# Kernel optimization log

Hardware: AMD Instinct MI355X
Metric: run time of the kernel (lower is better)

Reference implementation:

```python
import jax, jax.numpy as jnp
import numpy as np
import math

# LLaMA-7B-style int8 attention (torch-int Int8LlamaAttention)
B, S, HID, NH, HD = 2, 1024, 4096, 32, 128
THETA = 10000.0
# per-tensor quantization scales (as produced by from_float)
S_IN, S_W, S_B = 0.02, 0.01, 0.1
S_Q, S_K, S_V, S_O = 0.05, 0.05, 0.05, 0.05


def _rope_tables(position_ids):
    inv_freq = 1.0 / (THETA ** (jnp.arange(0, HD, 2, dtype=jnp.float32) / HD))
    freqs = position_ids.astype(jnp.float32)[..., None] * inv_freq  # [B,S,HD//2]
    emb = jnp.concatenate([freqs, freqs], axis=-1)  # [B,S,HD]
    return jnp.cos(emb)[:, None], jnp.sin(emb)[:, None]  # [B,1,S,HD]


def _rotate_half(x):
    return jnp.concatenate([-x[..., HD // 2:], x[..., :HD // 2]], axis=-1)


def _quant_i8(x):
    return jnp.clip(jnp.round(x), -128, 127).astype(jnp.int8)


def _w8a8b8o8(x_i8, w_i8, b_i8, alpha, beta):
    # int8 GEMM with int32 accumulation, fused dequant-requant to int8
    acc = jnp.einsum('bsk,nk->bsn', x_i8.astype(jnp.int32), w_i8.astype(jnp.int32))
    return _quant_i8(acc.astype(jnp.float32) * alpha + b_i8.astype(jnp.float32) * beta)


def setup_inputs() -> dict:
    key = jax.random.key(0)
    ks = jax.random.split(key, 9)
    ri8 = lambda k, shp: jax.random.randint(k, shp, -127, 128, dtype=jnp.int8)
    return {
        'hidden_states': jax.random.normal(ks[0], (B, S, HID), jnp.float32),
        'position_ids': jnp.broadcast_to(jnp.arange(S, dtype=jnp.int32), (B, S)),
        'w_q': ri8(ks[1], (HID, HID)),
        'w_k': ri8(ks[2], (HID, HID)),
        'w_v': ri8(ks[3], (HID, HID)),
        'w_o': ri8(ks[4], (HID, HID)),
        'b_q': ri8(ks[5], (HID,)),
        'b_k': ri8(ks[6], (HID,)),
        'b_v': ri8(ks[7], (HID,)),
        'b_o': jax.random.normal(ks[8], (HID,), jnp.float32) * 0.01,
    }


def reference(hidden_states, position_ids, w_q, w_k, w_v, w_o, b_q, b_k, b_v, b_o):
    # quantize activations, run int8 q/k/v projections (W8A8B8O8Linear)
    x_i8 = _quant_i8(hidden_states / S_IN)
    q = _w8a8b8o8(x_i8, w_q, b_q, S_IN * S_W / S_Q, S_B / S_Q)
    k = _w8a8b8o8(x_i8, w_k, b_k, S_IN * S_W / S_K, S_B / S_K)
    v = _w8a8b8o8(x_i8, w_v, b_v, S_IN * S_W / S_V, S_B / S_V)
    to_heads = lambda t: t.reshape(B, S, NH, HD).transpose(0, 2, 1, 3)  # [B,NH,S,HD]
    q, k, v = to_heads(q), to_heads(k), to_heads(v)
    # RoPE applied on dequantized int8 values, requantized for the int8 qk bmm
    cos, sin = _rope_tables(position_ids)
    qf, kf = q.astype(jnp.float32), k.astype(jnp.float32)
    q_i8 = _quant_i8(qf * cos + _rotate_half(qf) * sin)
    k_i8 = _quant_i8(kf * cos + _rotate_half(kf) * sin)
    # BMM_S8T_S8N_F32T: int8 QK^T -> fp32 with scale s_q*s_k, then /sqrt(d)
    attn = jnp.einsum('bhsd,bhtd->bhst', q_i8.astype(jnp.int32), k_i8.astype(jnp.int32))
    attn = attn.astype(jnp.float32) * (S_Q * S_K) / math.sqrt(HD)
    # NOTE: source never applies the attention mask (`attn_weights = attn_weights`)
    p = jax.nn.softmax(attn, axis=-1)
    # probs quantized to int8 with scale 1/127 for BMM_S8T_S8N_S8T
    p_i8 = _quant_i8(p * 127.0)
    ctx = jnp.einsum('bhst,bhtd->bhsd', p_i8.astype(jnp.int32), v.astype(jnp.int32))
    ctx_i8 = _quant_i8(ctx.astype(jnp.float32) * ((1.0 / 127.0) * S_V / S_O))
    ctx_i8 = ctx_i8.transpose(0, 2, 1, 3).reshape(B, S, HID)
    # W8A8BFP32OFP32 o_proj: int8 GEMM, fp32 output + fp32 bias
    out = jnp.einsum('bsk,nk->bsn', ctx_i8.astype(jnp.int32), w_o.astype(jnp.int32))
    return out.astype(jnp.float32) * (S_O * S_W) + b_o
```

## Files before the change

### kernel.cpp

```cpp
#include <hip/hip_runtime.h>
#include <hip/hip_bf16.h>
#include <cstdint>
#include <cstddef>

typedef int v4i __attribute__((ext_vector_type(4)));

#define NH 32
#define HD 128
#define SEQ 1024
#define HID 4096
#define BB 2
#define BKB 128

__device__ __forceinline__ signed char quant_i8(float x) {
    float r = rintf(x);
    r = fminf(fmaxf(r, -128.0f), 127.0f);
    return (signed char)r;
}

#define GLOAD_LDS16(g, l) \
    __builtin_amdgcn_global_load_lds((const __attribute__((address_space(1))) void*)(g), \
                                     (__attribute__((address_space(3))) void*)(l), 16, 0, 0)

__global__ __launch_bounds__(256) void pack4_i8_kernel(
    const int* __restrict__ s0, const int* __restrict__ s1,
    const int* __restrict__ s2, const int* __restrict__ s3,
    signed char* __restrict__ d0, signed char* __restrict__ d1,
    signed char* __restrict__ d2, signed char* __restrict__ d3, int n4)
{
    int i = blockIdx.x * 256 + threadIdx.x;
    int which = i / n4;
    int idx = i - which * n4;
    const int* src = (which == 0) ? s0 : (which == 1) ? s1 : (which == 2) ? s2 : s3;
    signed char* dst = (which == 0) ? d0 : (which == 1) ? d1 : (which == 2) ? d2 : d3;
    int4 v = ((const int4*)src)[idx];
    char4 c;
    c.x = (signed char)v.x; c.y = (signed char)v.y;
    c.z = (signed char)v.z; c.w = (signed char)v.w;
    ((char4*)dst)[idx] = c;
}

__global__ __launch_bounds__(256) void quant_x_kernel(const float* __restrict__ src,
                                                      signed char* __restrict__ dst, int n4) {
    int i = blockIdx.x * 256 + threadIdx.x;
    if (i >= n4) return;
    float4 v = ((const float4*)src)[i];
    char4 c;
    c.x = quant_i8(v.x * 50.0f);
    c.y = quant_i8(v.y * 50.0f);
    c.z = quant_i8(v.z * 50.0f);
    c.w = quant_i8(v.w * 50.0f);
    ((char4*)dst)[i] = c;
}

template<bool F32OUT>
__device__ __forceinline__ void gemm_core_db(
    const signed char* __restrict__ A, const signed char* __restrict__ Bw,
    const void* __restrict__ bias, void* __restrict__ outp,
    int m0, int n0, int N, int K, float alpha, float beta)
{
    __shared__ __align__(16) signed char sA[2 * 128 * BKB];
    __shared__ __align__(16) signed char sB[2 * 128 * BKB];

    const int t    = threadIdx.x;
    const int w    = t >> 6;
    const int lane = t & 63;
    const int lm   = lane & 15;
    const int quad = lane >> 4;
    const int wm   = (w >> 1) * 64;
    const int wn   = (w & 1) * 64;

    int srow[4], skc[4];
    #pragma unroll
    for (int p = 0; p < 4; p++) {
        int si = t + 256 * p;
        int row = si >> 3;
        srow[p] = row;
        skc[p] = ((si & 7) - (row >> 1)) & 7;
    }

    v4i acc[4][4] = {};

    #pragma unroll
    for (int p = 0; p < 4; p++) {
        GLOAD_LDS16(A  + (size_t)(m0 + srow[p]) * K + skc[p] * 16, sA + t * 16 + p * 4096);
        GLOAD_LDS16(Bw + (size_t)(n0 + srow[p]) * K + skc[p] * 16, sB + t * 16 + p * 4096);
    }

    int buf = 0;
    for (int k0 = 0; k0 < K; k0 += BKB) {
        __syncthreads();

        if (k0 + BKB < K) {
            int nb = buf ^ 1;
            #pragma unroll
            for (int p = 0; p < 4; p++) {
                GLOAD_LDS16(A  + (size_t)(m0 + srow[p]) * K + k0 + BKB + skc[p] * 16,
                            sA + nb * 16384 + t * 16 + p * 4096);
                GLOAD_LDS16(Bw + (size_t)(n0 + srow[p]) * K + k0 + BKB + skc[p] * 16,
                            sB + nb * 16384 + t * 16 + p * 4096);
            }
        }

        const signed char* pA = sA + buf * 16384;
        const signed char* pB = sB + buf * 16384;
        #pragma unroll
        for (int ks = 0; ks < 2; ks++) {
            v4i af[4], bf[4];
            #pragma unroll
            for (int i = 0; i < 4; i++) {
                int row = wm + 16 * i + lm;
                int slot = (ks * 4 + quad + (lm >> 1)) & 7;
                af[i] = *(const v4i*)(pA + row * BKB + slot * 16);
            }
            #pragma unroll
            for (int j = 0; j < 4; j++) {
                int row = wn + 16 * j + lm;
                int slot = (ks * 4 + quad + (lm >> 1)) & 7;
                bf[j] = *(const v4i*)(pB + row * BKB + slot * 16);
            }
            #pragma unroll
            for (int i = 0; i < 4; i++)
                #pragma unroll
                for (int j = 0; j < 4; j++)
                    acc[i][j] = __builtin_amdgcn_mfma_i32_16x16x64_i8(af[i], bf[j], acc[i][j], 0, 0, 0);
        }
        buf ^= 1;
    }

    const int orow = quad * 4;
    #pragma unroll
    for (int i = 0; i < 4; i++) {
        #pragma unroll
        for (int j = 0; j < 4; j++) {
            #pragma unroll
            for (int r = 0; r < 4; r++) {
                int row = m0 + wm + 16 * i + orow + r;
                int col = n0 + wn + 16 * j + lm;
                float v = (float)acc[i][j][r];
                if (F32OUT) {
                    ((float*)outp)[(size_t)row * N + col] = v * alpha + ((const float*)bias)[col];
                } else {
                    float q = v * alpha + (float)((const int*)bias)[col] * beta;
                    ((signed char*)outp)[(size_t)row * N + col] = quant_i8(q);
                }
            }
        }
    }
}

__global__ __launch_bounds__(256) void gemm_qkv(
    const signed char* __restrict__ x8,
    const signed char* __restrict__ wq, const signed char* __restrict__ wk,
    const signed char* __restrict__ wv,
    const int* __restrict__ bq, const int* __restrict__ bk, const int* __restrict__ bv,
    signed char* __restrict__ q8, signed char* __restrict__ k8, signed char* __restrict__ v8)
{
    const int nblk = blockIdx.x;
    const int which = nblk >> 5;
    const int n0 = (nblk & 31) * 128;
    const int m0 = blockIdx.y * 128;
    const signed char* Bw = (which == 0) ? wq : (which == 1) ? wk : wv;
    const int* bias = (which == 0) ? bq : (which == 1) ? bk : bv;
    signed char* outp = (which == 0) ? q8 : (which == 1) ? k8 : v8;
    gemm_core_db<false>(x8, Bw, bias, outp, m0, n0, HID, HID, 0.004f, 2.0f);
}

__global__ __launch_bounds__(256) void gemm_o(
    const signed char* __restrict__ c8, const signed char* __restrict__ wo,
    const float* __restrict__ bo, float* __restrict__ outp)
{
    gemm_core_db<true>(c8, wo, bo, outp, blockIdx.y * 128, blockIdx.x * 128,
                       HID, HID, 0.0005f, 0.0f);
}

__global__ __launch_bounds__(128) void rope_kernel(
    const int* __restrict__ pos_ids, signed char* __restrict__ q,
    signed char* __restrict__ k, const signed char* __restrict__ v,
    signed char* __restrict__ vt)
{
    const int bid = blockIdx.x;
    const int sg = bid & 127;
    const int h  = (bid >> 7) & (NH - 1);
    const int b  = bid >> 12;
    const int d  = threadIdx.x;
    const int s0 = sg * 8;
    const int bh = b * NH + h;

    float inv = expf(-(float)(2 * (d & 63)) * (9.210340371976184f / 128.0f));

    float qd[8], qp[8], kd[8], kp[8];
    signed char vd[8];
    int pos[8];
    size_t base[8];
    #pragma unroll
    for (int i = 0; i < 8; i++) {
        int s = s0 + i;
        base[i] = ((size_t)(b * SEQ + s) * NH + h) * (size_t)HD;
        pos[i] = pos_ids[b * SEQ + s];
        qd[i] = (float)q[base[i] + d];
        qp[i] = (float)q[base[i] + (d ^ 64)];
        kd[i] = (float)k[base[i] + d];
        kp[i] = (float)k[base[i] + (d ^ 64)];
        vd[i] = v[base[i] + d];
    }
    __syncthreads();

    union { signed char c[8]; int2 i2; } vu;
    #pragma unroll
    for (int i = 0; i < 8; i++) {
        float freq = (float)pos[i] * inv;
        float cs = cosf(freq), sn = sinf(freq);
        float rotq = (d < 64) ? -qp[i] : qp[i];
        float rotk = (d < 64) ? -kp[i] : kp[i];
        q[base[i] + d] = quant_i8(qd[i] * cs + rotq * sn);
        k[base[i] + d] = quant_i8(kd[i] * cs + rotk * sn);
        vu.c[i] = vd[i];
    }
    *(int2*)(vt + ((size_t)(bh * HD + d)) * SEQ + s0) = vu.i2;
}

__global__ __launch_bounds__(256) void attn_kernel(
    const signed char* __restrict__ q, const signed char* __restrict__ k,
    const signed char* __restrict__ vt, signed char* __restrict__ ctx)
{
    __shared__ __align__(16) signed char p8[32 * 1040];
    __shared__ float red[128];

    const int w    = threadIdx.x >> 6;
    const int lane = threadIdx.x & 63;
    const int bid  = blockIdx.x;
    const int mt   = bid & 31;
    const int bh   = bid >> 5;
    const int b    = bh >> 5, h = bh & 31;
    const int m0   = mt * 32;
    const int lm   = lane & 15;
    const int quad = lane >> 4;

    const float SCALE = 0.0025f / 11.313708498984761f;
    const float LOG2E = 1.4426950408889634f;

    const signed char* qb_base = q + ((size_t)(b * SEQ + m0 + lm) * NH + h) * (size_t)HD + quad * 16;
    v4i qb0 = *(const v4i*)qb_base;
    v4i qb1 = *(const v4i*)(qb_base + 64);
    const signed char* qb_base2 = qb_base + (size_t)16 * NH * HD;
    v4i qb2 = *(const v4i*)qb_base2;
    v4i qb3 = *(const v4i*)(qb_base2 + 64);

    float vals0[16][4], vals1[16][4];
    #pragma unroll
    for (int j = 0; j < 16; j++) {
        int t0 = w * 256 + j * 16;
        const signed char* kb = k + ((size_t)(b * SEQ + t0 + lm) * NH + h) * (size_t)HD + quad * 16;
        v4i a0 = *(const v4i*)kb;
        v4i a1 = *(const v4i*)(kb + 64);
        v4i acc0 = {}, acc1 = {};
        acc0 = __builtin_amdgcn_mfma_i32_16x16x64_i8(a0, qb0, acc0, 0, 0, 0);
        acc0 = __builtin_amdgcn_mfma_i32_16x16x64_i8(a1, qb1, acc0, 0, 0, 0);
        acc1 = __builtin_amdgcn_mfma_i32_16x16x64_i8(a0, qb2, acc1, 0, 0, 0);
        acc1 = __builtin_amdgcn_mfma_i32_16x16x64_i8(a1, qb3, acc1, 0, 0, 0);
        #pragma unroll
        for (int r = 0; r < 4; r++) {
            vals0[j][r] = (float)acc0[r] * SCALE;
            vals1[j][r] = (float)acc1[r] * SCALE;
        }
    }

    float mx0 = vals0[0][0], mx1 = vals1[0][0];
    #pragma unroll
    for (int j = 0; j < 16; j++)
        #pragma unroll
        for (int r = 0; r < 4; r++) {
            mx0 = fmaxf(mx0, vals0[j][r]);
            mx1 = fmaxf(mx1, vals1[j][r]);
        }
    mx0 = fmaxf(mx0, __shfl_xor(mx0, 16)); mx0 = fmaxf(mx0, __shfl_xor(mx0, 32));
    mx1 = fmaxf(mx1, __shfl_xor(mx1, 16)); mx1 = fmaxf(mx1, __shfl_xor(mx1, 32));
    if (lane < 16) { red[w * 16 + lane] = mx0; red[64 + w * 16 + lane] = mx1; }
    __syncthreads();
    mx0 = fmaxf(fmaxf(red[lm], red[16 + lm]), fmaxf(red[32 + lm], red[48 + lm]));
    mx1 = fmaxf(fmaxf(red[64 + lm], red[80 + lm]), fmaxf(red[96 + lm], red[112 + lm]));

    float sum0 = 0.f, sum1 = 0.f;
    #pragma unroll
    for (int j = 0; j < 16; j++)
        #pragma unroll
        for (int r = 0; r < 4; r++) {
            vals0[j][r] = exp2f((vals0[j][r] - mx0) * LOG2E); sum0 += vals0[j][r];
            vals1[j][r] = exp2f((vals1[j][r] - mx1) * LOG2E); sum1 += vals1[j][r];
        }
    sum0 += __shfl_xor(sum0, 16); sum0 += __shfl_xor(sum0, 32);
    sum1 += __shfl_xor(sum1, 16); sum1 += __shfl_xor(sum1, 32);
    __syncthreads();
    if (lane < 16) { red[w * 16 + lane] = sum0; red[64 + w * 16 + lane] = sum1; }
    __syncthreads();
    sum0 = (red[lm] + red[16 + lm]) + (red[32 + lm] + red[48 + lm]);
    sum1 = (red[64 + lm] + red[80 + lm]) + (red[96 + lm] + red[112 + lm]);
    float sf0 = 127.0f / sum0, sf1 = 127.0f / sum1;

    #pragma unroll
    for (int j = 0; j < 16; j++) {
        union { signed char cc[4]; int ii; } u0, u1;
        #pragma unroll
        for (int r = 0; r < 4; r++) {
            u0.cc[r] = quant_i8(vals0[j][r] * sf0);
            u1.cc[r] = quant_i8(vals1[j][r] * sf1);
        }
        *(int*)(p8 + lm * 1040 + w * 256 + j * 16 + quad * 4) = u0.ii;
        *(int*)(p8 + (16 + lm) * 1040 + w * 256 + j * 16 + quad * 4) = u1.ii;
    }
    __syncthreads();

    const int lkb = quad * 16;
    v4i accp0[2] = {}, accp1[2] = {};
    for (int kk = 0; kk < SEQ; kk += 64) {
        v4i af0 = *(const v4i*)(p8 + lm * 1040 + kk + lkb);
        v4i af1 = *(const v4i*)(p8 + (16 + lm) * 1040 + kk + lkb);
        #pragma unroll
        for (int j = 0; j < 2; j++) {
            int col = w * 32 + j * 16;
            v4i vb = *(const v4i*)(vt + ((size_t)(bh * HD + col + lm)) * (size_t)SEQ + kk + lkb);
            accp0[j] = __builtin_amdgcn_mfma_i32_16x16x64_i8(af0, vb, accp0[j], 0, 0, 0);
            accp1[j] = __builtin_amdgcn_mfma_i32_16x16x64_i8(af1, vb, accp1[j], 0, 0, 0);
        }
    }
    #pragma unroll
    for (int j = 0; j < 2; j++) {
        #pragma unroll
        for (int r = 0; r < 4; r++) {
            int row = quad * 4 + r;
            int col = w * 32 + j * 16 + lm;
            ctx[((size_t)(b * SEQ + m0 + row) * NH + h) * (size_t)HD + col] =
                quant_i8((float)accp0[j][r] * (1.0f / 127.0f));
            ctx[((size_t)(b * SEQ + m0 + 16 + row) * NH + h) * (size_t)HD + col] =
                quant_i8((float)accp1[j][r] * (1.0f / 127.0f));
        }
    }
}

extern "C" void kernel_launch(void* const* d_in, const int* in_sizes, int n_in,
                              void* d_out, int out_size, void* d_ws, size_t ws_size,
                              hipStream_t stream)
{
    const float* hidden = (const float*)d_in[0];
    const int* pos_ids  = (const int*)d_in[1];
    const int* w_q = (const int*)d_in[2];
    const int* w_k = (const int*)d_in[3];
    const int* w_v = (const int*)d_in[4];
    const int* w_o = (const int*)d_in[5];
    const int* b_q = (const int*)d_in[6];
    const int* b_k = (const int*)d_in[7];
    const int* b_v = (const int*)d_in[8];
    const float* b_o = (const float*)d_in[9];
    float* out = (float*)d_out;

    char* ws = (char*)d_ws;
    const size_t WSZ = (size_t)HID * HID;
    signed char* wq8 = (signed char*)ws;
    signed char* wk8 = wq8 + WSZ;
    signed char* wv8 = wk8 + WSZ;
    signed char* wo8 = wv8 + WSZ;
    signed char* x8  = wo8 + WSZ;
    const size_t ASZ = (size_t)BB * SEQ * HID;
    signed char* q8  = x8 + ASZ;
    signed char* k8  = q8 + ASZ;
    signed char* v8  = k8 + ASZ;
    signed char* vt8 = v8 + ASZ;
    signed char* c8  = vt8 + ASZ;

    int wn4 = HID * HID / 4;
    pack4_i8_kernel<<<4 * wn4 / 256, 256, 0, stream>>>(w_q, w_k, w_v, w_o,
                                                       wq8, wk8, wv8, wo8, wn4);
    int xn4 = (int)(ASZ / 4);
    quant_x_kernel<<<xn4 / 256, 256, 0, stream>>>(hidden, x8, xn4);

    gemm_qkv<<<dim3(96, 16), 256, 0, stream>>>(x8, wq8, wk8, wv8, b_q, b_k, b_v,
                                               q8, k8, v8);

    rope_kernel<<<BB * NH * (SEQ / 8), 128, 0, stream>>>(pos_ids, q8, k8, v8, vt8);
    attn_kernel<<<BB * NH * (SEQ / 32), 256, 0, stream>>>(q8, k8, vt8, c8);

    gemm_o<<<dim3(32, 16), 256, 0, stream>>>(c8, wo8, b_o, out);
}
```

Measured before the change: 544.0 us.

## Retune LDS swizzles, add XCD-aware block mapping, setprio and fast sincos

```diff
diff --git a/kernel.cpp b/kernel.cpp
--- a/kernel.cpp
+++ b/kernel.cpp
@@ -29,8 +29,8 @@
     signed char* __restrict__ d2, signed char* __restrict__ d3, int n4)
 {
     int i = blockIdx.x * 256 + threadIdx.x;
-    int which = i / n4;
-    int idx = i - which * n4;
+    int which = i >> 22;
+    int idx = i & ((1 << 22) - 1);
     const int* src = (which == 0) ? s0 : (which == 1) ? s1 : (which == 2) ? s2 : s3;
     signed char* dst = (which == 0) ? d0 : (which == 1) ? d1 : (which == 2) ? d2 : d3;
     int4 v = ((const int4*)src)[idx];
@@ -76,7 +76,7 @@
         int si = t + 256 * p;
         int row = si >> 3;
         srow[p] = row;
-        skc[p] = ((si & 7) - (row >> 1)) & 7;
+        skc[p] = ((si & 7) - row) & 7;
     }
 
     v4i acc[4][4] = {};
@@ -106,17 +106,16 @@
         const signed char* pB = sB + buf * 16384;
         #pragma unroll
         for (int ks = 0; ks < 2; ks++) {
+            const int slot = (ks * 4 + quad + lm) & 7;
             v4i af[4], bf[4];
             #pragma unroll
             for (int i = 0; i < 4; i++) {
                 int row = wm + 16 * i + lm;
-                int slot = (ks * 4 + quad + (lm >> 1)) & 7;
                 af[i] = *(const v4i*)(pA + row * BKB + slot * 16);
             }
             #pragma unroll
             for (int j = 0; j < 4; j++) {
                 int row = wn + 16 * j + lm;
-                int slot = (ks * 4 + quad + (lm >> 1)) & 7;
                 bf[j] = *(const v4i*)(pB + row * BKB + slot * 16);
             }
             #pragma unroll
@@ -156,10 +155,15 @@
     const int* __restrict__ bq, const int* __restrict__ bk, const int* __restrict__ bv,
     signed char* __restrict__ q8, signed char* __restrict__ k8, signed char* __restrict__ v8)
 {
-    const int nblk = blockIdx.x;
-    const int which = nblk >> 5;
-    const int n0 = (nblk & 31) * 128;
-    const int m0 = blockIdx.y * 128;
+    const int id  = blockIdx.x + 96 * blockIdx.y;
+    const int xcd = id & 7;
+    const int j   = id >> 3;
+    const int g   = j >> 6;
+    const int r   = j & 63;
+    const int nb  = xcd * 12 + g * 4 + (r & 3);
+    const int m0  = (r >> 2) * 128;
+    const int which = nb >> 5;
+    const int n0  = (nb & 31) * 128;
     const signed char* Bw = (which == 0) ? wq : (which == 1) ? wk : wv;
     const int* bias = (which == 0) ? bq : (which == 1) ? bk : bv;
     signed char* outp = (which == 0) ? q8 : (which == 1) ? k8 : v8;
@@ -170,8 +174,12 @@
     const signed char* __restrict__ c8, const signed char* __restrict__ wo,
     const float* __restrict__ bo, float* __restrict__ outp)
 {
-    gemm_core_db<true>(c8, wo, bo, outp, blockIdx.y * 128, blockIdx.x * 128,
-                       HID, HID, 0.0005f, 0.0f);
+    const int id  = blockIdx.x + 32 * blockIdx.y;
+    const int xcd = id & 7;
+    const int j   = id >> 3;
+    const int nb  = xcd * 4 + (j & 3);
+    const int m0  = (j >> 2) * 128;
+    gemm_core_db<true>(c8, wo, bo, outp, m0, nb * 128, HID, HID, 0.0005f, 0.0f);
 }
 
 __global__ __launch_bounds__(128) void rope_kernel(
@@ -210,7 +218,8 @@
     #pragma unroll
     for (int i = 0; i < 8; i++) {
         float freq = (float)pos[i] * inv;
-        float cs = cosf(freq), sn = sinf(freq);
+        float cs, sn;
+        __sincosf(freq, &sn, &cs);
         float rotq = (d < 64) ? -qp[i] : qp[i];
         float rotk = (d < 64) ? -kp[i] : kp[i];
         q[base[i] + d] = quant_i8(qd[i] * cs + rotq * sn);
@@ -255,10 +264,12 @@
         v4i a0 = *(const v4i*)kb;
         v4i a1 = *(const v4i*)(kb + 64);
         v4i acc0 = {}, acc1 = {};
+        __builtin_amdgcn_s_setprio(1);
         acc0 = __builtin_amdgcn_mfma_i32_16x16x64_i8(a0, qb0, acc0, 0, 0, 0);
         acc0 = __builtin_amdgcn_mfma_i32_16x16x64_i8(a1, qb1, acc0, 0, 0, 0);
         acc1 = __builtin_amdgcn_mfma_i32_16x16x64_i8(a0, qb2, acc1, 0, 0, 0);
         acc1 = __builtin_amdgcn_mfma_i32_16x16x64_i8(a1, qb3, acc1, 0, 0, 0);
+        __builtin_amdgcn_s_setprio(0);
         #pragma unroll
         for (int r = 0; r < 4; r++) {
             vals0[j][r] = (float)acc0[r] * SCALE;
@@ -306,23 +317,25 @@
             u0.cc[r] = quant_i8(vals0[j][r] * sf0);
             u1.cc[r] = quant_i8(vals1[j][r] * sf1);
         }
-        *(int*)(p8 + lm * 1040 + w * 256 + j * 16 + quad * 4) = u0.ii;
-        *(int*)(p8 + (16 + lm) * 1040 + w * 256 + j * 16 + quad * 4) = u1.ii;
-    }
-    __syncthreads();
-
-    const int lkb = quad * 16;
+        int ch = (((w * 16 + j) + 4 * lm) & 63) * 16 + quad * 4;
+        *(int*)(p8 + lm * 1040 + ch) = u0.ii;
+        *(int*)(p8 + (16 + lm) * 1040 + ch) = u1.ii;
+    }
+    __syncthreads();
+
     v4i accp0[2] = {}, accp1[2] = {};
     for (int kk = 0; kk < SEQ; kk += 64) {
-        v4i af0 = *(const v4i*)(p8 + lm * 1040 + kk + lkb);
-        v4i af1 = *(const v4i*)(p8 + (16 + lm) * 1040 + kk + lkb);
-        #pragma unroll
-        for (int j = 0; j < 2; j++) {
-            int col = w * 32 + j * 16;
-            v4i vb = *(const v4i*)(vt + ((size_t)(bh * HD + col + lm)) * (size_t)SEQ + kk + lkb);
-            accp0[j] = __builtin_amdgcn_mfma_i32_16x16x64_i8(af0, vb, accp0[j], 0, 0, 0);
-            accp1[j] = __builtin_amdgcn_mfma_i32_16x16x64_i8(af1, vb, accp1[j], 0, 0, 0);
-        }
+        int ph = (((kk >> 4) + quad) + 4 * lm) & 63;
+        v4i af0 = *(const v4i*)(p8 + lm * 1040 + ph * 16);
+        v4i af1 = *(const v4i*)(p8 + (16 + lm) * 1040 + ph * 16);
+        v4i vb0 = *(const v4i*)(vt + ((size_t)(bh * HD + w * 32 + lm)) * (size_t)SEQ + kk + quad * 16);
+        v4i vb1 = *(const v4i*)(vt + ((size_t)(bh * HD + w * 32 + 16 + lm)) * (size_t)SEQ + kk + quad * 16);
+        __builtin_amdgcn_s_setprio(1);
+        accp0[0] = __builtin_amdgcn_mfma_i32_16x16x64_i8(af0, vb0, accp0[0], 0, 0, 0);
+        accp1[0] = __builtin_amdgcn_mfma_i32_16x16x64_i8(af1, vb0, accp1[0], 0, 0, 0);
+        accp0[1] = __builtin_amdgcn_mfma_i32_16x16x64_i8(af0, vb1, accp0[1], 0, 0, 0);
+        accp1[1] = __builtin_amdgcn_mfma_i32_16x16x64_i8(af1, vb1, accp1[1], 0, 0, 0);
+        __builtin_amdgcn_s_setprio(0);
     }
     #pragma unroll
     for (int j = 0; j < 2; j++) {
```

Result: no change. 549.3 us (+1.0%).
